# Optimization experiments

Hardware: AMD Instinct MI355X
Metric: run time of the kernel (lower is better)

## Reference

```python
import jax, jax.numpy as jnp
import numpy as np

E, R, K, D, B = 100000, 1000, 200, 256, 65536  # entities, relations, bundle heads, emb dim, batch


def setup_inputs() -> dict:
    key = jax.random.key(0)
    ks = jax.random.split(key, 12)
    ent_emb = jax.random.normal(ks[0], (E, D), dtype=jnp.float32)
    ent_emb = ent_emb / jnp.linalg.norm(ent_emb, axis=1, keepdims=True)  # xavier + L2 row-normalize
    heads = jax.random.normal(ks[1], (K, D), dtype=jnp.float32)
    heads = heads / jnp.linalg.norm(heads, axis=1, keepdims=True)  # normalize_vvrel_embeddings
    bases = jax.random.normal(ks[2], (R, 2, D), dtype=jnp.float32)
    bases = bases / jnp.linalg.norm(bases, axis=2, keepdims=True)  # normalize_all_rows
    rel2head = jax.random.randint(ks[3], (R,), 0, K)              # r_id2_vrr[rel][0] -> head idx
    rel2mult = jnp.where(jax.random.bernoulli(ks[4], 0.5, (R,)), 1.0, -1.0).astype(jnp.float32)  # r_id2_vrr[rel][1]
    return {
        'pos_h': jax.random.randint(ks[5], (B,), 0, E),
        'pos_t': jax.random.randint(ks[6], (B,), 0, E),
        'pos_r': jax.random.randint(ks[7], (B,), 0, R),
        'neg_h': jax.random.randint(ks[8], (B,), 0, E),
        'neg_t': jax.random.randint(ks[9], (B,), 0, E),
        'neg_r': jax.random.randint(ks[10], (B,), 0, R),
        'ent_emb': ent_emb, 'heads': heads, 'bases': bases,
        'rel2head': rel2head, 'rel2mult': rel2mult,
    }


def _transint_scores(pos_h, pos_t, pos_r, neg_h, neg_t, ent_emb, heads, bases, rel2head, rel2mult):
    # vvrel_embedding_func: head embedding scaled by +-1 multiplier
    r_e = heads[rel2head[pos_r]] * rel2mult[pos_r][:, None]           # [B, D]
    pos_sub = ent_emb[pos_h] + r_e - ent_emb[pos_t]                    # [B, D]
    neg_sub = ent_emb[neg_h] + r_e - ent_emb[neg_t]                    # [B, D] (note: uses pos_r_e, as in source)
    sub = jnp.concatenate([pos_sub, neg_sub], axis=0)                  # [2B, D]
    A = bases[jnp.concatenate([pos_r, pos_r], axis=0)]                 # [2B, 2, D] per-sample basis (comb_mats gather)
    # ATA and closed-form 2x2 inverse (module's `inverse`)
    ATA = jnp.einsum('bkd,bld->bkl', A, A)                             # [2B, 2, 2]
    a, b = ATA[:, 0, 0], ATA[:, 0, 1]
    c, d = ATA[:, 1, 0], ATA[:, 1, 1]
    det = a * d - b * c
    safe_det = jnp.where(det != 0, det, 1.0)
    inv_reg = jnp.stack([jnp.stack([d, -b], -1), jnp.stack([-c, a], -1)], -2) / safe_det[:, None, None]
    inv_fb = jnp.eye(2, dtype=ATA.dtype)[None] / a[:, None, None]      # fallback when det == 0
    ATA_inv = jnp.where((det != 0)[:, None, None], inv_reg, inv_fb)    # [2B, 2, 2]
    # P @ sub with P = I - A^T (A A^T)^{-1} A, applied without materializing P
    Asub = jnp.einsum('bkd,bd->bk', A, sub)                            # [2B, 2]
    proj = sub - jnp.einsum('bkd,bk->bd', A, jnp.einsum('bkl,bl->bk', ATA_inv, Asub))
    score = jnp.sum(proj ** 2, axis=1)                                 # L1_flag = False -> squared L2
    nb = pos_h.shape[0]
    return score[:nb], score[nb:]


def reference(pos_h, pos_t, pos_r, neg_h, neg_t, neg_r, ent_emb, heads, bases, rel2head, rel2mult):
    return _transint_scores(pos_h, pos_t, pos_r, neg_h, neg_t, ent_emb, heads, bases, rel2head, rel2mult)
```

## Files before the change

### kernel.cpp

```cpp
#include <hip/hip_runtime.h>

#define D 256
#define D4 (D/4)

__device__ inline float dot4(const float4 u, const float4 v) {
    return u.x*v.x + u.y*v.y + u.z*v.z + u.w*v.w;
}

__device__ inline float wsum(float v) {
    #pragma unroll
    for (int off = 32; off > 0; off >>= 1)
        v += __shfl_xor(v, off, 64);
    return v;
}

__global__ __launch_bounds__(256) void transint_relprep(
    const float* __restrict__ heads,
    const float* __restrict__ bases,
    const int*   __restrict__ rel2head,
    const float* __restrict__ rel2mult,
    float*       __restrict__ rel_f,
    float*       __restrict__ par_buf,
    int R)
{
    const int r    = (blockIdx.x * blockDim.x + threadIdx.x) >> 6;
    const int lane = threadIdx.x & 63;
    if (r >= R) return;

    const int   hd   = rel2head[r];
    const float mult = rel2mult[r];
    const float4* hrow = (const float4*)(heads + (size_t)hd * D);
    const float4* arow = (const float4*)(bases + (size_t)r * 2 * D);

    float4 a0 = arow[lane];
    float4 a1 = arow[D4 + lane];
    float4 re = hrow[lane];
    re.x *= mult; re.y *= mult; re.z *= mult; re.w *= mult;

    float aa = wsum(dot4(a0, a0));
    float ab = wsum(dot4(a0, a1));
    float dd = wsum(dot4(a1, a1));

    float det = aa * dd - ab * ab;
    float m00, m01, m11;
    if (det != 0.0f) {
        float inv = 1.0f / det;
        m00 = dd * inv; m01 = -ab * inv; m11 = aa * inv;
    } else {
        float inv = 1.0f / aa;
        m00 = inv; m01 = 0.0f; m11 = inv;
    }
    float t00 = aa * m00 + ab * m01;
    float t01 = aa * m01 + ab * m11;
    float t10 = ab * m00 + dd * m01;
    float t11 = ab * m01 + dd * m11;
    float q00 = 2.f * m00 - (m00 * t00 + m01 * t10);
    float q01 = 2.f * m01 - (m00 * t01 + m01 * t11);
    float q11 = 2.f * m11 - (m01 * t01 + m11 * t11);

    float c00  = sqrtf(aa);
    float ic00 = (c00 > 0.f) ? 1.f / c00 : 0.f;
    float4 u0;
    u0.x = a0.x * ic00; u0.y = a0.y * ic00; u0.z = a0.z * ic00; u0.w = a0.w * ic00;
    float c10 = ab * ic00;
    float4 v;
    v.x = a1.x - c10 * u0.x; v.y = a1.y - c10 * u0.y;
    v.z = a1.z - c10 * u0.z; v.w = a1.w - c10 * u0.w;
    float vv   = wsum(dot4(v, v));
    float c11  = sqrtf(vv);
    float ic11 = (c11 > 0.f) ? 1.f / c11 : 0.f;
    float4 u1;
    u1.x = v.x * ic11; u1.y = v.y * ic11; u1.z = v.z * ic11; u1.w = v.w * ic11;

    float s00 = c00*c00*q00 + 2.f*c00*c10*q01 + c10*c10*q11;
    float s01 = c00*c11*q01 + c10*c11*q11;
    float s11 = c11*c11*q11;

    float4* rf = (float4*)(rel_f + (size_t)r * 3 * D);
    rf[lane]          = u0;
    rf[D4 + lane]     = u1;
    rf[2 * D4 + lane] = re;

    if (lane == 0) {
        float* p = par_buf + (size_t)r * 4;
        p[0] = s00; p[1] = s01; p[2] = s11; p[3] = 0.f;
    }
}

__global__ __launch_bounds__(256) void transint_main_f32(
    const int*   __restrict__ pos_h,
    const int*   __restrict__ pos_t,
    const int*   __restrict__ pos_r,
    const int*   __restrict__ neg_h,
    const int*   __restrict__ neg_t,
    const float* __restrict__ ent,
    const float* __restrict__ rel_f,
    const float* __restrict__ par_buf,
    float*       __restrict__ out,
    int nB)
{
    const int wave = (blockIdx.x * blockDim.x + threadIdx.x) >> 6;
    const int lane = threadIdx.x & 63;
    const int g    = lane >> 4;
    const int gl   = lane & 15;
    const int b    = wave * 4 + g;
    if (b >= nB) return;

    const int r = pos_r[b];
    const float4* ph = (const float4*)ent + (size_t)pos_h[b] * D4;
    const float4* pt = (const float4*)ent + (size_t)pos_t[b] * D4;
    const float4* nh = (const float4*)ent + (size_t)neg_h[b] * D4;
    const float4* nt = (const float4*)ent + (size_t)neg_t[b] * D4;
    const float4* rb = (const float4*)rel_f + (size_t)r * (3 * D4);

    float4 H[4], T[4], X[4], Y[4], U0[4], U1[4], RE[4];
    #pragma unroll
    for (int c = 0; c < 4; ++c) {
        const int fi = gl + 16 * c;
        H[c]  = ph[fi];
        T[c]  = pt[fi];
        X[c]  = nh[fi];
        Y[c]  = nt[fi];
        U0[c] = rb[fi];
        U1[c] = rb[D4 + fi];
        RE[c] = rb[2 * D4 + fi];
    }

    float pp0 = 0.f, pp1 = 0.f, ssp = 0.f;
    float pn0 = 0.f, pn1 = 0.f, ssn = 0.f;

    #pragma unroll
    for (int c = 0; c < 4; ++c) {
        #define ACC(comp) {                                   \
            float ps = H[c].comp - T[c].comp + RE[c].comp;    \
            float ns = X[c].comp - Y[c].comp + RE[c].comp;    \
            pp0 = fmaf(U0[c].comp, ps, pp0);                  \
            pp1 = fmaf(U1[c].comp, ps, pp1);                  \
            ssp = fmaf(ps, ps, ssp);                          \
            pn0 = fmaf(U0[c].comp, ns, pn0);                  \
            pn1 = fmaf(U1[c].comp, ns, pn1);                  \
            ssn = fmaf(ns, ns, ssn); }
        ACC(x) ACC(y) ACC(z) ACC(w)
        #undef ACC
    }

    #pragma unroll
    for (int off = 8; off > 0; off >>= 1) {
        pp0 += __shfl_xor(pp0, off, 64);
        pp1 += __shfl_xor(pp1, off, 64);
        ssp += __shfl_xor(ssp, off, 64);
        pn0 += __shfl_xor(pn0, off, 64);
        pn1 += __shfl_xor(pn1, off, 64);
        ssn += __shfl_xor(ssn, off, 64);
    }

    if (gl == 0) {
        const float* par = par_buf + (size_t)r * 4;
        const float s00 = par[0], s01 = par[1], s11 = par[2];
        out[b]      = ssp - (s00*pp0*pp0 + 2.f*s01*pp0*pp1 + s11*pp1*pp1);
        out[nB + b] = ssn - (s00*pn0*pn0 + 2.f*s01*pn0*pn1 + s11*pn1*pn1);
    }
}

extern "C" void kernel_launch(void* const* d_in, const int* in_sizes, int n_in,
                              void* d_out, int out_size, void* d_ws, size_t ws_size,
                              hipStream_t stream) {
    const int*   pos_h    = (const int*)  d_in[0];
    const int*   pos_t    = (const int*)  d_in[1];
    const int*   pos_r    = (const int*)  d_in[2];
    const int*   neg_h    = (const int*)  d_in[3];
    const int*   neg_t    = (const int*)  d_in[4];
    const float* ent_emb  = (const float*)d_in[6];
    const float* heads    = (const float*)d_in[7];
    const float* bases    = (const float*)d_in[8];
    const int*   rel2head = (const int*)  d_in[9];
    const float* rel2mult = (const float*)d_in[10];
    float* out = (float*)d_out;

    const int nB = in_sizes[0];
    const int R  = in_sizes[9];

    float* rel_f   = (float*)d_ws;
    float* par_buf = rel_f + (size_t)R * 3 * D;

    {
        dim3 grid((R + 3) / 4);
        transint_relprep<<<grid, dim3(256), 0, stream>>>(
            heads, bases, rel2head, rel2mult, rel_f, par_buf, R);
    }
    {
        dim3 grid((nB + 15) / 16);
        transint_main_f32<<<grid, dim3(256), 0, stream>>>(
            pos_h, pos_t, pos_r, neg_h, neg_t,
            ent_emb, rel_f, par_buf, out, nB);
    }
}
```

Before: 197.0 us.

## Convert entity and relation tables to fp16 before the gather kernel

The prep kernel now converts the whole entity embedding table to fp16 on every call, alongside the relation prep, and also stores the relation vectors in fp16. The main kernel then gathers half-width rows with 16-byte loads and accumulates in fp32. This halves the bytes moved by the random row gathers, which dominate the main kernel. In exchange, each call adds a full streaming read and write of the entity table, and fp16 rounding of the inputs adds error to the scores.

```diff
diff --git a/kernel.cpp b/kernel.cpp
--- a/kernel.cpp
+++ b/kernel.cpp
@@ -2,6 +2,13 @@
 
 #define D 256
 #define D4 (D/4)
+#define ROW_U2 64
+#define ROW_I4 32
+
+typedef _Float16 f16;
+
+union H4 { uint2 u; f16 h[4]; };
+union H8 { int4  i; f16 h[8]; };
 
 __device__ inline float dot4(const float4 u, const float4 v) {
     return u.x*v.x + u.y*v.y + u.z*v.z + u.w*v.w;
@@ -14,17 +21,29 @@
     return v;
 }
 
-__global__ __launch_bounds__(256) void transint_relprep(
-    const float* __restrict__ heads,
-    const float* __restrict__ bases,
-    const int*   __restrict__ rel2head,
-    const float* __restrict__ rel2mult,
-    float*       __restrict__ rel_f,
-    float*       __restrict__ par_buf,
-    int R)
+__global__ __launch_bounds__(256) void transint_prep(
+    const float*  __restrict__ ent,
+    const float*  __restrict__ heads,
+    const float*  __restrict__ bases,
+    const int*    __restrict__ rel2head,
+    const float*  __restrict__ rel2mult,
+    uint2*        __restrict__ ent_h,
+    uint2*        __restrict__ rel_h,
+    float*        __restrict__ par_buf,
+    int E, int R)
 {
-    const int r    = (blockIdx.x * blockDim.x + threadIdx.x) >> 6;
+    const int wave = (blockIdx.x * blockDim.x + threadIdx.x) >> 6;
     const int lane = threadIdx.x & 63;
+
+    if (wave < E) {
+        float4 v = ((const float4*)ent)[(size_t)wave * D4 + lane];
+        H4 p;
+        p.h[0] = (f16)v.x; p.h[1] = (f16)v.y;
+        p.h[2] = (f16)v.z; p.h[3] = (f16)v.w;
+        ent_h[(size_t)wave * ROW_U2 + lane] = p.u;
+        return;
+    }
+    const int r = wave - E;
     if (r >= R) return;
 
     const int   hd   = rel2head[r];
@@ -76,10 +95,17 @@
     float s01 = c00*c11*q01 + c10*c11*q11;
     float s11 = c11*c11*q11;
 
-    float4* rf = (float4*)(rel_f + (size_t)r * 3 * D);
-    rf[lane]          = u0;
-    rf[D4 + lane]     = u1;
-    rf[2 * D4 + lane] = re;
+    uint2* rb = rel_h + (size_t)r * (3 * ROW_U2);
+    H4 pu0, pu1, pre;
+    pu0.h[0] = (f16)u0.x; pu0.h[1] = (f16)u0.y;
+    pu0.h[2] = (f16)u0.z; pu0.h[3] = (f16)u0.w;
+    pu1.h[0] = (f16)u1.x; pu1.h[1] = (f16)u1.y;
+    pu1.h[2] = (f16)u1.z; pu1.h[3] = (f16)u1.w;
+    pre.h[0] = (f16)re.x; pre.h[1] = (f16)re.y;
+    pre.h[2] = (f16)re.z; pre.h[3] = (f16)re.w;
+    rb[lane]              = pu0.u;
+    rb[ROW_U2 + lane]     = pu1.u;
+    rb[2 * ROW_U2 + lane] = pre.u;
 
     if (lane == 0) {
         float* p = par_buf + (size_t)r * 4;
@@ -87,14 +113,14 @@
     }
 }
 
-__global__ __launch_bounds__(256) void transint_main_f32(
+__global__ __launch_bounds__(256) void transint_main_f16(
     const int*   __restrict__ pos_h,
     const int*   __restrict__ pos_t,
     const int*   __restrict__ pos_r,
     const int*   __restrict__ neg_h,
     const int*   __restrict__ neg_t,
-    const float* __restrict__ ent,
-    const float* __restrict__ rel_f,
+    const int4*  __restrict__ ent_h,
+    const int4*  __restrict__ rel_h,
     const float* __restrict__ par_buf,
     float*       __restrict__ out,
     int nB)
@@ -107,41 +133,52 @@
     if (b >= nB) return;
 
     const int r = pos_r[b];
-    const float4* ph = (const float4*)ent + (size_t)pos_h[b] * D4;
-    const float4* pt = (const float4*)ent + (size_t)pos_t[b] * D4;
-    const float4* nh = (const float4*)ent + (size_t)neg_h[b] * D4;
-    const float4* nt = (const float4*)ent + (size_t)neg_t[b] * D4;
-    const float4* rb = (const float4*)rel_f + (size_t)r * (3 * D4);
-
-    float4 H[4], T[4], X[4], Y[4], U0[4], U1[4], RE[4];
-    #pragma unroll
-    for (int c = 0; c < 4; ++c) {
-        const int fi = gl + 16 * c;
-        H[c]  = ph[fi];
-        T[c]  = pt[fi];
-        X[c]  = nh[fi];
-        Y[c]  = nt[fi];
-        U0[c] = rb[fi];
-        U1[c] = rb[D4 + fi];
-        RE[c] = rb[2 * D4 + fi];
+    const int4* ph = ent_h + (size_t)pos_h[b] * ROW_I4;
+    const int4* pt = ent_h + (size_t)pos_t[b] * ROW_I4;
+    const int4* nh = ent_h + (size_t)neg_h[b] * ROW_I4;
+    const int4* nt = ent_h + (size_t)neg_t[b] * ROW_I4;
+    const int4* rb = rel_h + (size_t)r * (3 * ROW_I4);
+
+    int4 Hq[2], Tq[2], Xq[2], Yq[2], U0q[2], U1q[2], REq[2];
+    #pragma unroll
+    for (int c = 0; c < 2; ++c) {
+        const int idx = 2 * gl + c;
+        Hq[c]  = ph[idx];
+        Tq[c]  = pt[idx];
+        Xq[c]  = nh[idx];
+        Yq[c]  = nt[idx];
+        U0q[c] = rb[idx];
+        U1q[c] = rb[ROW_I4 + idx];
+        REq[c] = rb[2 * ROW_I4 + idx];
     }
 
     float pp0 = 0.f, pp1 = 0.f, ssp = 0.f;
     float pn0 = 0.f, pn1 = 0.f, ssn = 0.f;
 
     #pragma unroll
-    for (int c = 0; c < 4; ++c) {
-        #define ACC(comp) {                                   \
-            float ps = H[c].comp - T[c].comp + RE[c].comp;    \
-            float ns = X[c].comp - Y[c].comp + RE[c].comp;    \
-            pp0 = fmaf(U0[c].comp, ps, pp0);                  \
-            pp1 = fmaf(U1[c].comp, ps, pp1);                  \
-            ssp = fmaf(ps, ps, ssp);                          \
-            pn0 = fmaf(U0[c].comp, ns, pn0);                  \
-            pn1 = fmaf(U1[c].comp, ns, pn1);                  \
-            ssn = fmaf(ns, ns, ssn); }
-        ACC(x) ACC(y) ACC(z) ACC(w)
-        #undef ACC
+    for (int c = 0; c < 2; ++c) {
+        H8 hh, tt, xx, yy, ua, ub, rr;
+        hh.i = Hq[c];  tt.i = Tq[c];
+        xx.i = Xq[c];  yy.i = Yq[c];
+        ua.i = U0q[c]; ub.i = U1q[c]; rr.i = REq[c];
+        #pragma unroll
+        for (int j = 0; j < 8; ++j) {
+            const float h  = (float)hh.h[j];
+            const float t  = (float)tt.h[j];
+            const float x  = (float)xx.h[j];
+            const float y  = (float)yy.h[j];
+            const float a  = (float)ua.h[j];
+            const float b2 = (float)ub.h[j];
+            const float re = (float)rr.h[j];
+            const float ps = h - t + re;
+            const float ns = x - y + re;
+            pp0 = fmaf(a,  ps, pp0);
+            pp1 = fmaf(b2, ps, pp1);
+            ssp = fmaf(ps, ps, ssp);
+            pn0 = fmaf(a,  ns, pn0);
+            pn1 = fmaf(b2, ns, pn1);
+            ssn = fmaf(ns, ns, ssn);
+        }
     }
 
     #pragma unroll
@@ -179,19 +216,23 @@
 
     const int nB = in_sizes[0];
     const int R  = in_sizes[9];
-
-    float* rel_f   = (float*)d_ws;
-    float* par_buf = rel_f + (size_t)R * 3 * D;
+    const int E  = in_sizes[6] / D;
+
+    uint2* ent_h   = (uint2*)d_ws;
+    uint2* rel_h   = (uint2*)((char*)d_ws + (size_t)E * 512);
+    float* par_buf = (float*)((char*)d_ws + (size_t)E * 512 + (size_t)R * 1536);
 
     {
-        dim3 grid((R + 3) / 4);
-        transint_relprep<<<grid, dim3(256), 0, stream>>>(
-            heads, bases, rel2head, rel2mult, rel_f, par_buf, R);
+        int waves = E + R;
+        dim3 grid((waves + 3) / 4);
+        transint_prep<<<grid, dim3(256), 0, stream>>>(
+            ent_emb, heads, bases, rel2head, rel2mult,
+            ent_h, rel_h, par_buf, E, R);
     }
     {
         dim3 grid((nB + 15) / 16);
-        transint_main_f32<<<grid, dim3(256), 0, stream>>>(
+        transint_main_f16<<<grid, dim3(256), 0, stream>>>(
             pos_h, pos_t, pos_r, neg_h, neg_t,
-            ent_emb, rel_f, par_buf, out, nB);
-    }
-}
+            (const int4*)ent_h, (const int4*)rel_h, par_buf, out, nB);
+    }
+}
```

New measurement: 207.3 us. +5.2%, slower.
